# Kernel optimization log

Hardware: AMD Instinct MI355X
Metric: run time of the kernel (lower is better)

## Reference

```python
import jax, jax.numpy as jnp
import numpy as np


def setup_inputs() -> dict:
    key = jax.random.key(0)
    k1, k2 = jax.random.split(key)
    C, H, W = 64, 1024, 1024
    NUM_SP = 2048
    x = jax.random.normal(k1, (C, H, W), dtype=jnp.float32)
    sp = jax.random.randint(k2, (H, W), 0, NUM_SP, dtype=jnp.int32)
    return {"x": x, "sp": sp, "num_segments": NUM_SP}


def reference(x, sp, num_segments):
    # x: [C, H, W], sp: [H, W] superpixel labels in [0, num_segments)
    C, H, W = x.shape
    N = H * W
    sp_flat = sp.reshape(N)                      # [N]
    x_flat = x.reshape(C, N).T                   # [N, C]
    # Per-superpixel, per-channel sums and pixel counts (single-pass segment reduce)
    sums = jax.ops.segment_sum(x_flat, sp_flat, num_segments=num_segments)   # [S, C]
    counts = jax.ops.segment_sum(jnp.ones((N,), dtype=x.dtype), sp_flat,
                                 num_segments=num_segments)                  # [S]
    means = sums / jnp.maximum(counts, 1.0)[:, None]                         # [S, C]
    # Broadcast each superpixel's mean back to its pixels
    out = means[sp_flat].T.reshape(C, H, W)
    return out
```

## Files before the change

kernel.cpp:

```cpp
#include <hip/hip_runtime.h>

#define NUM_SP 2048
#define CG 4
#define SUM_THREADS 1024
#define BCAST_THREADS 512
#define BCAST_CHUNKS 64


__global__ __launch_bounds__(256) void zero_kernel(float* ws, int n) {
    int i = blockIdx.x * 256 + threadIdx.x;
    int stride = gridDim.x * 256;
    for (; i < n; i += stride) ws[i] = 0.0f;
}

__global__ __launch_bounds__(256) void count_kernel(const int* __restrict__ sp,
                                                    float* __restrict__ counts, int N) {
    __shared__ int hist[NUM_SP];
    for (int i = threadIdx.x; i < NUM_SP; i += 256) hist[i] = 0;
    __syncthreads();
    int per = (N + gridDim.x - 1) / gridDim.x;
    int base = blockIdx.x * per;
    int end = base + per; if (end > N) end = N;
    for (int p = base + threadIdx.x; p < end; p += 256) {
        atomicAdd(&hist[sp[p]], 1);
    }
    __syncthreads();
    for (int i = threadIdx.x; i < NUM_SP; i += 256) {
        int c = hist[i];
        if (c) atomicAdd(&counts[i], (float)c);
    }
}

__global__ __launch_bounds__(SUM_THREADS, 8) void sum_kernel(
        const float* __restrict__ x, const int* __restrict__ sp,
        unsigned long long* __restrict__ outq,
        int N, int NG, int chunks, int use_partials, float scale) {
    __shared__ unsigned long long acc[NUM_SP * 2];
    for (int i = threadIdx.x; i < NUM_SP * 2; i += SUM_THREADS) acc[i] = 0ULL;
    __syncthreads();

    const int g = blockIdx.y;
    const int chunk = blockIdx.x;
    const int per = (N + chunks - 1) / chunks;
    const int base = chunk * per;
    int end = base + per; if (end > N) end = N;
    const float* xg = x + (size_t)g * CG * N;
    const float bsr = 8.0f * scale + 0.5f;

    int p = base + (int)threadIdx.x;
    for (; p + SUM_THREADS < end; p += 2 * SUM_THREADS) {
        int p2 = p + SUM_THREADS;
        int s0 = sp[p];
        int s1 = sp[p2];
        float v0a = xg[0 * N + p],  v1a = xg[0 * N + p2];
        float v0b = xg[1 * N + p],  v1b = xg[1 * N + p2];
        float v0c = xg[2 * N + p],  v1c = xg[2 * N + p2];
        float v0d = xg[3 * N + p],  v1d = xg[3 * N + p2];
        unsigned int a0 = (unsigned int)fmaf(v0a, scale, bsr);
        unsigned int b0 = (unsigned int)fmaf(v0b, scale, bsr);
        unsigned int c0 = (unsigned int)fmaf(v0c, scale, bsr);
        unsigned int d0 = (unsigned int)fmaf(v0d, scale, bsr);
        unsigned int a1 = (unsigned int)fmaf(v1a, scale, bsr);
        unsigned int b1 = (unsigned int)fmaf(v1b, scale, bsr);
        unsigned int c1 = (unsigned int)fmaf(v1c, scale, bsr);
        unsigned int d1 = (unsigned int)fmaf(v1d, scale, bsr);
        unsigned long long q00 = (unsigned long long)a0 | ((unsigned long long)b0 << 32);
        unsigned long long q01 = (unsigned long long)c0 | ((unsigned long long)d0 << 32);
        unsigned long long q10 = (unsigned long long)a1 | ((unsigned long long)b1 << 32);
        unsigned long long q11 = (unsigned long long)c1 | ((unsigned long long)d1 << 32);
        atomicAdd(&acc[(s0 << 1) + 0], q00);
        atomicAdd(&acc[(s0 << 1) + 1], q01);
        atomicAdd(&acc[(s1 << 1) + 0], q10);
        atomicAdd(&acc[(s1 << 1) + 1], q11);
    }
    for (; p < end; p += SUM_THREADS) {
        int s = sp[p];
        unsigned int a0 = (unsigned int)fmaf(xg[0 * N + p], scale, bsr);
        unsigned int b0 = (unsigned int)fmaf(xg[1 * N + p], scale, bsr);
        unsigned int c0 = (unsigned int)fmaf(xg[2 * N + p], scale, bsr);
        unsigned int d0 = (unsigned int)fmaf(xg[3 * N + p], scale, bsr);
        atomicAdd(&acc[(s << 1) + 0], (unsigned long long)a0 | ((unsigned long long)b0 << 32));
        atomicAdd(&acc[(s << 1) + 1], (unsigned long long)c0 | ((unsigned long long)d0 << 32));
    }
    __syncthreads();

    unsigned long long* dst = outq + (size_t)(use_partials ? (chunk * NG + g) : g) * (NUM_SP * 2);
    for (int i = threadIdx.x; i < NUM_SP * 2; i += SUM_THREADS) {
        unsigned long long v = acc[i];
        if (use_partials) dst[i] = v;
        else if (v) atomicAdd(&dst[i], v);
    }
}

__global__ __launch_bounds__(256) void mean_kernel(const unsigned long long* __restrict__ partq,
                                                   const float* __restrict__ counts,
                                                   float* __restrict__ means_gm,
                                                   int SC, int NG, int chunks, float scale) {
    int i = blockIdx.x * 256 + threadIdx.x;
    if (i >= SC) return;
    int s = i & (NUM_SP - 1);
    int c = i >> 11;
    int g = c >> 2, cl = c & 3, j = cl >> 1, half = cl & 1;
    unsigned long long fs = 0;
    for (int k = 0; k < chunks; ++k) {
        unsigned long long q = partq[(size_t)(k * NG + g) * (NUM_SP * 2) + (s << 1) + j];
        fs += (unsigned long long)(half ? (unsigned int)(q >> 32) : (unsigned int)q);
    }
    float cnt = counts[s];
    double sv = ((double)fs - (double)cnt * (double)(8.0f * scale)) / (double)scale;
    means_gm[((size_t)g * NUM_SP + s) * 4 + cl] = (float)(sv / fmax((double)cnt, 1.0));
}

__global__ __launch_bounds__(BCAST_THREADS, 8) void bcast_kernel(
        const int* __restrict__ sp, const float4* __restrict__ means_gm4,
        float* __restrict__ out, int N) {
    __shared__ float4 tbl[NUM_SP];
    const int g = blockIdx.y;
    for (int e = threadIdx.x; e < NUM_SP; e += BCAST_THREADS)
        tbl[e] = means_gm4[(size_t)g * NUM_SP + e];
    __syncthreads();

    const int per = (N + gridDim.x - 1) / gridDim.x;
    const int base = blockIdx.x * per;
    int end = base + per; if (end > N) end = N;
    float* o0 = out + (size_t)(g * CG + 0) * N;
    float* o1 = out + (size_t)(g * CG + 1) * N;
    float* o2 = out + (size_t)(g * CG + 2) * N;
    float* o3 = out + (size_t)(g * CG + 3) * N;

    int p = base + (int)threadIdx.x;
    for (; p + BCAST_THREADS < end; p += 2 * BCAST_THREADS) {
        int p2 = p + BCAST_THREADS;
        int s0 = sp[p];
        int s1 = sp[p2];
        float4 m0 = tbl[s0];
        float4 m1 = tbl[s1];
        o0[p] = m0.x; o1[p] = m0.y; o2[p] = m0.z; o3[p] = m0.w;
        o0[p2] = m1.x; o1[p2] = m1.y; o2[p2] = m1.z; o3[p2] = m1.w;
    }
    for (; p < end; p += BCAST_THREADS) {
        float4 m = tbl[sp[p]];
        o0[p] = m.x; o1[p] = m.y; o2[p] = m.z; o3[p] = m.w;
    }
}

extern "C" void kernel_launch(void* const* d_in, const int* in_sizes, int n_in,
                              void* d_out, int out_size, void* d_ws, size_t ws_size,
                              hipStream_t stream) {
    const float* x = (const float*)d_in[0];
    const int* sp = (const int*)d_in[1];
    const int N = in_sizes[1];
    const int C = in_sizes[0] / N;
    float* out = (float*)d_out;
    float* ws = (float*)d_ws;

    const int S = NUM_SP;
    const int SC = S * C;
    const int NG = C / CG;

    float* counts = ws;
    float* means = ws + S;
    unsigned long long* partq = (unsigned long long*)(ws + S + SC);

    size_t ws_floats = ws_size / sizeof(float);
    size_t avail = (ws_floats > (size_t)(S + SC)) ? ws_floats - (size_t)(S + SC) : 0;
    int chunks = (int)(avail / (size_t)SC);
    if (chunks > 32) chunks = 32;
    int use_partials = (chunks >= 4) ? 1 : 0;
    int grid_chunks = use_partials ? chunks : 32;
    float scale = use_partials ? 1048576.0f : 131072.0f;

    zero_kernel<<<64, 256, 0, stream>>>(ws, use_partials ? S : S + 2 * SC);
    count_kernel<<<256, 256, 0, stream>>>(sp, counts, N);
    dim3 g2(grid_chunks, NG);
    sum_kernel<<<g2, SUM_THREADS, 0, stream>>>(x, sp, partq, N, NG,
                                               grid_chunks, use_partials, scale);
    mean_kernel<<<(SC + 255) / 256, 256, 0, stream>>>(partq, counts, means, SC, NG,
                                                      use_partials ? grid_chunks : 1, scale);
    dim3 gb(BCAST_CHUNKS, NG);
    bcast_kernel<<<gb, BCAST_THREADS, 0, stream>>>(sp, (const float4*)means, out, N);
}
```

Measured before the change: 492.4 us.

## Pack three channels per 64-bit shared atomic with 21-bit fixed point

Lowers fixed-point precision so three channels fit into each 64-bit word instead of two. Each sum block now handles six channels (the last group four) with two atomics per pixel, so the 64 channels use 11 channel groups instead of 16. The chunk count rises to 46 to keep the grid filled. This cuts the number of LDS atomic operations per pixel and the partial-buffer traffic. In exchange the quantization scale is much coarser (2048 versus about a million), so mean accuracy drops, and each 21-bit field can overflow if a chunk's per-segment sums grow too large.

```diff
diff --git a/kernel.cpp b/kernel.cpp
--- a/kernel.cpp
+++ b/kernel.cpp
@@ -2,9 +2,13 @@
 
 #define NUM_SP 2048
 #define CG 4
+#define NG_SUM 11
 #define SUM_THREADS 1024
+#define SUM_CHUNKS 46
 #define BCAST_THREADS 512
 #define BCAST_CHUNKS 64
+#define FBITS 21
+#define FMASK ((1ULL << FBITS) - 1ULL)
 
 
 __global__ __launch_bounds__(256) void zero_kernel(float* ws, int n) {
@@ -31,60 +35,69 @@
     }
 }
 
-__global__ __launch_bounds__(SUM_THREADS, 8) void sum_kernel(
-        const float* __restrict__ x, const int* __restrict__ sp,
-        unsigned long long* __restrict__ outq,
-        int N, int NG, int chunks, int use_partials, float scale) {
-    __shared__ unsigned long long acc[NUM_SP * 2];
-    for (int i = threadIdx.x; i < NUM_SP * 2; i += SUM_THREADS) acc[i] = 0ULL;
-    __syncthreads();
-
-    const int g = blockIdx.y;
-    const int chunk = blockIdx.x;
-    const int per = (N + chunks - 1) / chunks;
-    const int base = chunk * per;
-    int end = base + per; if (end > N) end = N;
-    const float* xg = x + (size_t)g * CG * N;
-    const float bsr = 8.0f * scale + 0.5f;
-
+template <int CHN>
+__device__ __forceinline__ void sum_body(const float* __restrict__ xg,
+                                         const int* __restrict__ sp,
+                                         unsigned long long* __restrict__ acc,
+                                         int base, int end, int N,
+                                         float scale, float bsr) {
     int p = base + (int)threadIdx.x;
     for (; p + SUM_THREADS < end; p += 2 * SUM_THREADS) {
         int p2 = p + SUM_THREADS;
         int s0 = sp[p];
         int s1 = sp[p2];
-        float v0a = xg[0 * N + p],  v1a = xg[0 * N + p2];
-        float v0b = xg[1 * N + p],  v1b = xg[1 * N + p2];
-        float v0c = xg[2 * N + p],  v1c = xg[2 * N + p2];
-        float v0d = xg[3 * N + p],  v1d = xg[3 * N + p2];
-        unsigned int a0 = (unsigned int)fmaf(v0a, scale, bsr);
-        unsigned int b0 = (unsigned int)fmaf(v0b, scale, bsr);
-        unsigned int c0 = (unsigned int)fmaf(v0c, scale, bsr);
-        unsigned int d0 = (unsigned int)fmaf(v0d, scale, bsr);
-        unsigned int a1 = (unsigned int)fmaf(v1a, scale, bsr);
-        unsigned int b1 = (unsigned int)fmaf(v1b, scale, bsr);
-        unsigned int c1 = (unsigned int)fmaf(v1c, scale, bsr);
-        unsigned int d1 = (unsigned int)fmaf(v1d, scale, bsr);
-        unsigned long long q00 = (unsigned long long)a0 | ((unsigned long long)b0 << 32);
-        unsigned long long q01 = (unsigned long long)c0 | ((unsigned long long)d0 << 32);
-        unsigned long long q10 = (unsigned long long)a1 | ((unsigned long long)b1 << 32);
-        unsigned long long q11 = (unsigned long long)c1 | ((unsigned long long)d1 << 32);
+        float a[CHN], b[CHN];
+#pragma unroll
+        for (int c = 0; c < CHN; ++c) { a[c] = xg[c * N + p]; b[c] = xg[c * N + p2]; }
+        unsigned long long q00 = 0, q01 = 0, q10 = 0, q11 = 0;
+#pragma unroll
+        for (int c = 0; c < CHN; ++c) {
+            unsigned long long ua = (unsigned int)fmaf(a[c], scale, bsr);
+            unsigned long long ub = (unsigned int)fmaf(b[c], scale, bsr);
+            int sh = (c % 3) * FBITS;
+            if (c < 3) { q00 |= ua << sh; q10 |= ub << sh; }
+            else       { q01 |= ua << sh; q11 |= ub << sh; }
+        }
         atomicAdd(&acc[(s0 << 1) + 0], q00);
-        atomicAdd(&acc[(s0 << 1) + 1], q01);
+        if (CHN > 3) atomicAdd(&acc[(s0 << 1) + 1], q01);
         atomicAdd(&acc[(s1 << 1) + 0], q10);
-        atomicAdd(&acc[(s1 << 1) + 1], q11);
+        if (CHN > 3) atomicAdd(&acc[(s1 << 1) + 1], q11);
     }
     for (; p < end; p += SUM_THREADS) {
         int s = sp[p];
-        unsigned int a0 = (unsigned int)fmaf(xg[0 * N + p], scale, bsr);
-        unsigned int b0 = (unsigned int)fmaf(xg[1 * N + p], scale, bsr);
-        unsigned int c0 = (unsigned int)fmaf(xg[2 * N + p], scale, bsr);
-        unsigned int d0 = (unsigned int)fmaf(xg[3 * N + p], scale, bsr);
-        atomicAdd(&acc[(s << 1) + 0], (unsigned long long)a0 | ((unsigned long long)b0 << 32));
-        atomicAdd(&acc[(s << 1) + 1], (unsigned long long)c0 | ((unsigned long long)d0 << 32));
-    }
-    __syncthreads();
-
-    unsigned long long* dst = outq + (size_t)(use_partials ? (chunk * NG + g) : g) * (NUM_SP * 2);
+        unsigned long long q0 = 0, q1 = 0;
+#pragma unroll
+        for (int c = 0; c < CHN; ++c) {
+            unsigned long long u = (unsigned int)fmaf(xg[c * N + p], scale, bsr);
+            int sh = (c % 3) * FBITS;
+            if (c < 3) q0 |= u << sh; else q1 |= u << sh;
+        }
+        atomicAdd(&acc[(s << 1) + 0], q0);
+        if (CHN > 3) atomicAdd(&acc[(s << 1) + 1], q1);
+    }
+}
+
+__global__ __launch_bounds__(SUM_THREADS, 8) void sum_kernel(
+        const float* __restrict__ x, const int* __restrict__ sp,
+        unsigned long long* __restrict__ outq,
+        int N, int chunks, int use_partials, float scale, float bsr) {
+    __shared__ unsigned long long acc[NUM_SP * 2];
+    for (int i = threadIdx.x; i < NUM_SP * 2; i += SUM_THREADS) acc[i] = 0ULL;
+    __syncthreads();
+
+    const int gs = blockIdx.y;
+    const int chunk = blockIdx.x;
+    const int per = (N + chunks - 1) / chunks;
+    const int base = chunk * per;
+    int end = base + per; if (end > N) end = N;
+    const float* xg = x + (size_t)gs * 6 * N;
+
+    if (gs == NG_SUM - 1) sum_body<4>(xg, sp, acc, base, end, N, scale, bsr);
+    else                  sum_body<6>(xg, sp, acc, base, end, N, scale, bsr);
+    __syncthreads();
+
+    unsigned long long* dst = outq + (size_t)(use_partials ? (chunk * NG_SUM + gs) : gs)
+                                     * (NUM_SP * 2);
     for (int i = threadIdx.x; i < NUM_SP * 2; i += SUM_THREADS) {
         unsigned long long v = acc[i];
         if (use_partials) dst[i] = v;
@@ -95,20 +108,22 @@
 __global__ __launch_bounds__(256) void mean_kernel(const unsigned long long* __restrict__ partq,
                                                    const float* __restrict__ counts,
                                                    float* __restrict__ means_gm,
-                                                   int SC, int NG, int chunks, float scale) {
+                                                   int SC, int chunks, float scale) {
     int i = blockIdx.x * 256 + threadIdx.x;
     if (i >= SC) return;
     int s = i & (NUM_SP - 1);
     int c = i >> 11;
-    int g = c >> 2, cl = c & 3, j = cl >> 1, half = cl & 1;
+    int gs = c / 6;
+    int f = c - gs * 6;
+    int j = f / 3, sub = f - j * 3;
     unsigned long long fs = 0;
     for (int k = 0; k < chunks; ++k) {
-        unsigned long long q = partq[(size_t)(k * NG + g) * (NUM_SP * 2) + (s << 1) + j];
-        fs += (unsigned long long)(half ? (unsigned int)(q >> 32) : (unsigned int)q);
+        unsigned long long q = partq[(size_t)(k * NG_SUM + gs) * (NUM_SP * 2) + (s << 1) + j];
+        fs += (q >> (sub * FBITS)) & FMASK;
     }
     float cnt = counts[s];
-    double sv = ((double)fs - (double)cnt * (double)(8.0f * scale)) / (double)scale;
-    means_gm[((size_t)g * NUM_SP + s) * 4 + cl] = (float)(sv / fmax((double)cnt, 1.0));
+    double sv = ((double)fs - (double)cnt * (double)(6.0f * scale)) / (double)scale;
+    means_gm[((size_t)(c >> 2) * NUM_SP + s) * 4 + (c & 3)] = (float)(sv / fmax((double)cnt, 1.0));
 }
 
 __global__ __launch_bounds__(BCAST_THREADS, 8) void bcast_kernel(
@@ -162,20 +177,23 @@
     float* means = ws + S;
     unsigned long long* partq = (unsigned long long*)(ws + S + SC);
 
+    const size_t part_floats_per_chunk = (size_t)NG_SUM * NUM_SP * 2 * 2;
     size_t ws_floats = ws_size / sizeof(float);
     size_t avail = (ws_floats > (size_t)(S + SC)) ? ws_floats - (size_t)(S + SC) : 0;
-    int chunks = (int)(avail / (size_t)SC);
-    if (chunks > 32) chunks = 32;
-    int use_partials = (chunks >= 4) ? 1 : 0;
-    int grid_chunks = use_partials ? chunks : 32;
-    float scale = use_partials ? 1048576.0f : 131072.0f;
-
-    zero_kernel<<<64, 256, 0, stream>>>(ws, use_partials ? S : S + 2 * SC);
+    int chunks = (int)(avail / part_floats_per_chunk);
+    if (chunks > SUM_CHUNKS) chunks = SUM_CHUNKS;
+    int use_partials = (chunks >= 32) ? 1 : 0;
+    int grid_chunks = use_partials ? chunks : SUM_CHUNKS;
+    float scale = use_partials ? 2048.0f : 128.0f;
+    float bsr = 6.0f * scale + 0.5f;
+
+    zero_kernel<<<64, 256, 0, stream>>>(ws, use_partials ? S
+                                            : S + SC + (int)part_floats_per_chunk);
     count_kernel<<<256, 256, 0, stream>>>(sp, counts, N);
-    dim3 g2(grid_chunks, NG);
-    sum_kernel<<<g2, SUM_THREADS, 0, stream>>>(x, sp, partq, N, NG,
-                                               grid_chunks, use_partials, scale);
-    mean_kernel<<<(SC + 255) / 256, 256, 0, stream>>>(partq, counts, means, SC, NG,
+    dim3 g2(grid_chunks, NG_SUM);
+    sum_kernel<<<g2, SUM_THREADS, 0, stream>>>(x, sp, partq, N, grid_chunks,
+                                               use_partials, scale, bsr);
+    mean_kernel<<<(SC + 255) / 256, 256, 0, stream>>>(partq, counts, means, SC,
                                                       use_partials ? grid_chunks : 1, scale);
     dim3 gb(BCAST_CHUNKS, NG);
     bcast_kernel<<<gb, BCAST_THREADS, 0, stream>>>(sp, (const float4*)means, out, N);
```

After: 494.8 us. About the same (+0.5%).
